# Kernel optimization log

Measured on AMD Instinct MI355X. Metric: run time of the kernel, lower is better.

The kernel has to match this reference:

```python
import jax, jax.numpy as jnp
import numpy as np

H = 512
TEMPERATURE = 1.0


def setup_inputs() -> dict:
    key = jax.random.key(0)
    ks = jax.random.split(key, 9)
    B, Q, S = 4, 64, 1024
    scale = 1.0 / np.sqrt(H)
    return {
        "query": jax.random.normal(ks[0], (B, Q, H), jnp.float32),
        "key_": jax.random.normal(ks[1], (B, S, H), jnp.float32),
        "value": jax.random.normal(ks[2], (B, S, H), jnp.float32),
        "Wq": jax.random.normal(ks[3], (H, H), jnp.float32) * scale,
        "bq": jax.random.normal(ks[4], (H,), jnp.float32) * 0.01,
        "Wk": jax.random.normal(ks[5], (H, H), jnp.float32) * scale,
        "bk": jax.random.normal(ks[6], (H,), jnp.float32) * 0.01,
        "we": jax.random.normal(ks[7], (H,), jnp.float32) * scale,
        "be": jax.random.normal(ks[8], (), jnp.float32) * 0.01,
    }


def reference(query, key_, value, Wq, bq, Wk, bk, we, be):
    # query: [B,Q,H], key_/value: [B,S,H]
    qp = jnp.einsum("bqd,dh->bqh", query, Wq) + bq          # [B,Q,H]
    kp = jnp.einsum("bsd,dh->bsh", key_, Wk) + bk           # [B,S,H]
    attn_sum = jnp.tanh(qp[:, :, None, :] + kp[:, None, :, :])  # [B,Q,S,H]
    scores = (jnp.einsum("bqsh,h->bqs", attn_sum, we) + be) / TEMPERATURE
    weights = jax.nn.softmax(scores, axis=-1)               # [B,Q,S]
    context = jnp.einsum("bqs,bsh->bqh", weights, value)    # [B,Q,H]
    return context, weights
```

## Files before the change

### kernel.cpp

```cpp
#include <hip/hip_runtime.h>


constexpr int kB = 4;
constexpr int kQ = 64;
constexpr int kS = 1024;
constexpr int kH = 512;

typedef short bf16x8 __attribute__((ext_vector_type(8)));
typedef float f32x4 __attribute__((ext_vector_type(4)));

__device__ __forceinline__ unsigned bf16rtn_bits(float x) {
  unsigned u = __float_as_uint(x);
  u += 0x7FFFu + ((u >> 16) & 1u);
  return u;
}

__global__ __launch_bounds__(256) void convert_all(
    const float* __restrict__ Wk, const float* __restrict__ Wq,
    const float* __restrict__ key_, const float* __restrict__ query,
    unsigned short* __restrict__ Bhi, unsigned short* __restrict__ Blo,
    unsigned short* __restrict__ Xhi, unsigned short* __restrict__ Xlo) {
  __shared__ __align__(16) unsigned short LHi[128 * 40];
  __shared__ __align__(16) unsigned short LLo[128 * 40];
  const int bid = blockIdx.x;
  const int t = threadIdx.x;
  if (bid < 256) {
    const int gid = bid * 256 + t;
    const int c = gid & 63;
    const int g = (gid >> 6) & 3;
    const int kt = (gid >> 8) & 15;
    const int ct = (gid >> 12) & 7;
    const int mat = gid >> 15;
    const float* W = mat ? Wq : Wk;
    const float* src = W + (size_t)(kt * 32 + g * 8) * kH + ct * 64 + c;
    bf16x8 hv, lv;
#pragma unroll
    for (int j = 0; j < 8; j++) {
      float x = src[(size_t)j * kH];
      unsigned u = bf16rtn_bits(x);
      float hf = __uint_as_float(u & 0xFFFF0000u);
      unsigned v = bf16rtn_bits(x - hf);
      hv[j] = (short)(u >> 16);
      lv[j] = (short)(v >> 16);
    }
    *(bf16x8*)(Bhi + (size_t)gid * 8) = hv;
    *(bf16x8*)(Blo + (size_t)gid * 8) = lv;
    return;
  }
  const int xb = bid - 256;
  const int kt = xb & 15;
  const int rt = xb >> 4;
  const float* X = (rt < 32) ? (key_ + (size_t)rt * 128 * kH)
                             : (query + (size_t)(rt - 32) * 128 * kH);
  const int r = t >> 1, c0 = (t & 1) * 16;
  const float* src = X + (size_t)r * kH + kt * 32 + c0;
  bf16x8 hv0, hv1, lv0, lv1;
#pragma unroll
  for (int i = 0; i < 16; i++) {
    float x = src[i];
    unsigned u = bf16rtn_bits(x);
    float hf = __uint_as_float(u & 0xFFFF0000u);
    unsigned v = bf16rtn_bits(x - hf);
    if (i < 8) { hv0[i] = (short)(u >> 16); lv0[i] = (short)(v >> 16); }
    else       { hv1[i - 8] = (short)(u >> 16); lv1[i - 8] = (short)(v >> 16); }
  }
  *(bf16x8*)&LHi[r * 40 + c0] = hv0;
  *(bf16x8*)&LHi[r * 40 + c0 + 8] = hv1;
  *(bf16x8*)&LLo[r * 40 + c0] = lv0;
  *(bf16x8*)&LLo[r * 40 + c0 + 8] = lv1;
  __syncthreads();
  const size_t obase = (size_t)(rt * 16 + kt) * 512 * 8;
#pragma unroll
  for (int p = 0; p < 2; p++) {
    const int s = t + p * 256;
    const int rr = s & 127, g = s >> 7;
    *(uint4*)(Xhi + obase + (size_t)s * 8) = *(const uint4*)&LHi[rr * 40 + g * 8];
    *(uint4*)(Xlo + obase + (size_t)s * 8) = *(const uint4*)&LLo[rr * 40 + g * 8];
  }
}

__global__ __launch_bounds__(512) void proj_mfma(
    const unsigned short* __restrict__ Xhi, const unsigned short* __restrict__ Xlo,
    const unsigned short* __restrict__ Bhi, const unsigned short* __restrict__ Blo,
    const float* __restrict__ bk, const float* __restrict__ bq,
    float* __restrict__ Ek, float* __restrict__ Eq) {
  __shared__ __align__(16) unsigned short AhiL[2][4096];
  __shared__ __align__(16) unsigned short AloL[2][4096];
  __shared__ __align__(16) unsigned short BhiL[2][2048];
  __shared__ __align__(16) unsigned short BloL[2][2048];

  const int ct = blockIdx.x;
  const int rt = blockIdx.y;
  const int mat = (rt >= 32) ? 1 : 0;
  const float* bias = mat ? bq : bk;
  float* Y = mat ? (Eq + (size_t)(rt - 32) * 128 * kH)
                 : (Ek + (size_t)rt * 128 * kH);

  const int t = threadIdx.x;
  const unsigned short* ah_src = Xhi + ((size_t)(rt * 16) * 512 + t) * 8;
  const unsigned short* al_src = Xlo + ((size_t)(rt * 16) * 512 + t) * 8;
  const int bslot = t & 255;
  const unsigned short* b_src =
      ((t < 256) ? Bhi : Blo) + ((size_t)((mat * 8 + ct) * 16) * 256 + bslot) * 8;

  uint4 pah, pal, pb;
  auto gload = [&](int kt2) {
    pah = *(const uint4*)(ah_src + (size_t)kt2 * 512 * 8);
    pal = *(const uint4*)(al_src + (size_t)kt2 * 512 * 8);
    pb = *(const uint4*)(b_src + (size_t)kt2 * 256 * 8);
  };
  auto lwrite = [&](int buf) {
    *(uint4*)&AhiL[buf][t * 8] = pah;
    *(uint4*)&AloL[buf][t * 8] = pal;
    if (t < 256) *(uint4*)&BhiL[buf][bslot * 8] = pb;
    else         *(uint4*)&BloL[buf][bslot * 8] = pb;
  };

  const int l = t & 63, lg = l >> 4, lr = l & 15;
  const int wv = t >> 6, wm = wv & 3, wn = wv >> 2;

  f32x4 acc[2][2];
#pragma unroll
  for (int m = 0; m < 2; m++)
#pragma unroll
    for (int n = 0; n < 2; n++) acc[m][n] = {0.f, 0.f, 0.f, 0.f};

  gload(0);
  lwrite(0);
  __syncthreads();

  for (int kt2 = 0; kt2 < 16; kt2++) {
    if (kt2 < 15) gload(kt2 + 1);

    const unsigned short* Ah = AhiL[kt2 & 1];
    const unsigned short* Al = AloL[kt2 & 1];
    const unsigned short* Bh = BhiL[kt2 & 1];
    const unsigned short* Bl = BloL[kt2 & 1];
    bf16x8 ah[2], al[2], bh[2], bl[2];
#pragma unroll
    for (int m = 0; m < 2; m++) {
      const int off = (lg * 128 + wm * 32 + m * 16 + lr) * 8;
      ah[m] = *(const bf16x8*)(Ah + off);
      al[m] = *(const bf16x8*)(Al + off);
    }
#pragma unroll
    for (int n = 0; n < 2; n++) {
      const int off = (lg * 64 + wn * 32 + n * 16 + lr) * 8;
      bh[n] = *(const bf16x8*)(Bh + off);
      bl[n] = *(const bf16x8*)(Bl + off);
    }
#pragma unroll
    for (int m = 0; m < 2; m++)
#pragma unroll
      for (int n = 0; n < 2; n++) {
        acc[m][n] = __builtin_amdgcn_mfma_f32_16x16x32_bf16(ah[m], bh[n], acc[m][n], 0, 0, 0);
        acc[m][n] = __builtin_amdgcn_mfma_f32_16x16x32_bf16(al[m], bh[n], acc[m][n], 0, 0, 0);
        acc[m][n] = __builtin_amdgcn_mfma_f32_16x16x32_bf16(ah[m], bl[n], acc[m][n], 0, 0, 0);
      }

    if (kt2 < 15) {
      __syncthreads();
      lwrite((kt2 + 1) & 1);
      __syncthreads();
    }
  }

  const int col0 = ct * 64 + wn * 32 + lr;
  const float b0 = bias[col0];
  const float b1 = bias[col0 + 16];
#pragma unroll
  for (int m = 0; m < 2; m++) {
    const int row0 = wm * 32 + m * 16 + lg * 4;
#pragma unroll
    for (int jj = 0; jj < 4; jj++) {
      float* y = Y + (size_t)(row0 + jj) * kH;
      y[col0]      = __expf(2.f * (acc[m][0][jj] + b0));
      y[col0 + 16] = __expf(2.f * (acc[m][1][jj] + b1));
    }
  }
}

__global__ __launch_bounds__(256) void score_kernel(
    const float* __restrict__ Eq, const float* __restrict__ Ek,
    const float* __restrict__ we, float* __restrict__ sraw) {
  __shared__ __align__(16) float EkL[2][64 * 64];

  const int qt = blockIdx.x, st = blockIdx.y, b = blockIdx.z;
  const int t = threadIdx.x, lane = t & 63;
  const int wvu = __builtin_amdgcn_readfirstlane(t >> 6);
  const int s0 = st * 64;
  const int q0g = b * kQ + qt * 8;
  const int qA = wvu * 2;

  const float4* we4 = (const float4*)we;
  float4 u0 = we4[lane * 2], u1 = we4[lane * 2 + 1];
  float wsum = u0.x + u0.y + u0.z + u0.w + u1.x + u1.y + u1.z + u1.w;
#pragma unroll
  for (int off = 32; off; off >>= 1) wsum += __shfl_xor(wsum, off);

  const float4* qa4 = (const float4*)(Eq + (size_t)(q0g + qA) * kH);
  const float4* qb4 = (const float4*)(Eq + (size_t)(q0g + qA + 1) * kH);

  const int er = t >> 4;
  const int ej = t & 15;
  const float* ekg = Ek + (size_t)(b * kS + s0 + er) * kH + ej * 4;
  float4 pk[4];
  auto gload = [&](int c) {
#pragma unroll
    for (int i = 0; i < 4; i++)
      pk[i] = *(const float4*)(ekg + (size_t)(16 * i) * kH + c * 64);
  };
  auto lwrite = [&](int buf) {
#pragma unroll
    for (int i = 0; i < 4; i++) {
      const int row = er + 16 * i;
      *(float4*)(&EkL[buf][row * 64 + ((ej ^ (row & 15)) << 2)]) = pk[i];
    }
  };

  gload(0);
  lwrite(0);
  __syncthreads();

  float accA = 0.f, accB = 0.f;
  const int sw = lane & 15;

  for (int c = 0; c < 8; c++) {
    if (c < 7) gload(c + 1);
    const float* ekb = &EkL[c & 1][lane * 64];
#pragma unroll 4
    for (int g = 0; g < 16; g++) {
      float4 ek = *(const float4*)(ekb + ((g ^ sw) << 2));
      float4 w = we4[c * 16 + g];
      float4 qa = qa4[c * 16 + g];
      float4 qb = qb4[c * 16 + g];
      {
        float a1 = fmaf(qa.x, ek.x, 1.f), b1 = fmaf(qa.y, ek.y, 1.f);
        float n1 = fmaf(w.y, a1, w.x * b1);
        accA = fmaf(n1, __builtin_amdgcn_rcpf(a1 * b1), accA);
        float a2 = fmaf(qa.z, ek.z, 1.f), b2 = fmaf(qa.w, ek.w, 1.f);
        float n2 = fmaf(w.w, a2, w.z * b2);
        accA = fmaf(n2, __builtin_amdgcn_rcpf(a2 * b2), accA);
      }
      {
        float a1 = fmaf(qb.x, ek.x, 1.f), b1 = fmaf(qb.y, ek.y, 1.f);
        float n1 = fmaf(w.y, a1, w.x * b1);
        accB = fmaf(n1, __builtin_amdgcn_rcpf(a1 * b1), accB);
        float a2 = fmaf(qb.z, ek.z, 1.f), b2 = fmaf(qb.w, ek.w, 1.f);
        float n2 = fmaf(w.w, a2, w.z * b2);
        accB = fmaf(n2, __builtin_amdgcn_rcpf(a2 * b2), accB);
      }
    }
    if (c < 7) {
      __syncthreads();
      lwrite((c + 1) & 1);
      __syncthreads();
    }
  }

  sraw[(size_t)(q0g + qA + 0) * kS + s0 + lane] = fmaf(-2.f, accA, wsum);
  sraw[(size_t)(q0g + qA + 1) * kS + s0 + lane] = fmaf(-2.f, accB, wsum);
}

__global__ __launch_bounds__(256) void ctx_fused(
    const float* __restrict__ sraw, const float* __restrict__ value,
    float* __restrict__ wout, float* __restrict__ ctx) {
  __shared__ __align__(16) float wt[4][1024];
  __shared__ __align__(16) float parts[4][4][128];
  const int bid = blockIdx.x;
  const int qc = bid >> 4, b = (bid >> 2) & 3, hc = bid & 3;
  const int t = threadIdx.x, wv = t >> 6, lane = t & 63;
  const int grow = b * kQ + qc * 4 + wv;

  const float4* row4 = (const float4*)(sraw + (size_t)grow * kS);
  float4 v[4];
#pragma unroll
  for (int j = 0; j < 4; j++) v[j] = row4[lane + 64 * j];
  float m = -1e30f;
#pragma unroll
  for (int j = 0; j < 4; j++)
    m = fmaxf(m, fmaxf(fmaxf(v[j].x, v[j].y), fmaxf(v[j].z, v[j].w)));
#pragma unroll
  for (int off = 32; off; off >>= 1) m = fmaxf(m, __shfl_xor(m, off));
  float sum = 0.f;
#pragma unroll
  for (int j = 0; j < 4; j++) {
    v[j].x = __expf(v[j].x - m); v[j].y = __expf(v[j].y - m);
    v[j].z = __expf(v[j].z - m); v[j].w = __expf(v[j].w - m);
    sum += v[j].x + v[j].y + v[j].z + v[j].w;
  }
#pragma unroll
  for (int off = 32; off; off >>= 1) sum += __shfl_xor(sum, off);
  const float inv = 1.f / sum;
  float4* wrow = (float4*)&wt[wv][0];
  float4* gw = (float4*)(wout + (size_t)grow * kS);
#pragma unroll
  for (int j = 0; j < 4; j++) {
    v[j].x *= inv; v[j].y *= inv; v[j].z *= inv; v[j].w *= inv;
    wrow[lane + 64 * j] = v[j];
    if (hc == 0) gw[lane + 64 * j] = v[j];
  }
  __syncthreads();

  const float* vbase =
      value + ((size_t)b * kS + wv * 256) * kH + hc * 128 + lane * 2;
  float2 acc[4];
#pragma unroll
  for (int q = 0; q < 4; q++) acc[q] = {0.f, 0.f};
#pragma unroll 2
  for (int s4 = 0; s4 < 64; s4++) {
    float4 wq[4];
#pragma unroll
    for (int q = 0; q < 4; q++)
      wq[q] = *(const float4*)&wt[q][wv * 256 + s4 * 4];
#pragma unroll
    for (int u = 0; u < 4; u++) {
      const float2 vv = *(const float2*)(vbase + (size_t)(s4 * 4 + u) * kH);
      const float w0 = ((const float*)&wq[0])[u];
      const float w1 = ((const float*)&wq[1])[u];
      const float w2 = ((const float*)&wq[2])[u];
      const float w3 = ((const float*)&wq[3])[u];
      acc[0].x = fmaf(w0, vv.x, acc[0].x); acc[0].y = fmaf(w0, vv.y, acc[0].y);
      acc[1].x = fmaf(w1, vv.x, acc[1].x); acc[1].y = fmaf(w1, vv.y, acc[1].y);
      acc[2].x = fmaf(w2, vv.x, acc[2].x); acc[2].y = fmaf(w2, vv.y, acc[2].y);
      acc[3].x = fmaf(w3, vv.x, acc[3].x); acc[3].y = fmaf(w3, vv.y, acc[3].y);
    }
  }
#pragma unroll
  for (int q = 0; q < 4; q++)
    *(float2*)&parts[wv][q][lane * 2] = acc[q];
  __syncthreads();

  const int q = t >> 6, hp = t & 63;
  float2 r = {0.f, 0.f};
#pragma unroll
  for (int w = 0; w < 4; w++) {
    const float2 p2 = *(const float2*)&parts[w][q][hp * 2];
    r.x += p2.x; r.y += p2.y;
  }
  *(float2*)(ctx + (size_t)(b * kQ + qc * 4 + q) * kH + hc * 128 + hp * 2) = r;
}

extern "C" void kernel_launch(void* const* d_in, const int* in_sizes, int n_in,
                              void* d_out, int out_size, void* d_ws,
                              size_t ws_size, hipStream_t stream) {
  const float* query = (const float*)d_in[0];
  const float* key_  = (const float*)d_in[1];
  const float* value = (const float*)d_in[2];
  const float* Wq    = (const float*)d_in[3];
  const float* bq    = (const float*)d_in[4];
  const float* Wk    = (const float*)d_in[5];
  const float* bk    = (const float*)d_in[6];
  const float* we    = (const float*)d_in[7];

  float* ctx  = (float*)d_out;
  float* wout = (float*)d_out + (size_t)kB * kQ * kH;

  float* Eq = (float*)d_ws;
  float* Ek = Eq + (size_t)kB * kQ * kH;
  unsigned short* Bhi =
      (unsigned short*)((char*)d_ws + (size_t)(kB * kQ * kH + kB * kS * kH) * 4);
  unsigned short* Blo = Bhi + (size_t)2 * 8 * 16 * 256 * 8;
  unsigned short* Xhi = Blo + (size_t)2 * 8 * 16 * 256 * 8;
  unsigned short* Xlo = Xhi + (size_t)34 * 16 * 512 * 8;
  float* sraw = (float*)(Xlo + (size_t)34 * 16 * 512 * 8);

  convert_all<<<800, 256, 0, stream>>>(Wk, Wq, key_, query, Bhi, Blo, Xhi, Xlo);
  proj_mfma<<<dim3(8, 34), 512, 0, stream>>>(Xhi, Xlo, Bhi, Blo, bk, bq, Ek, Eq);
  score_kernel<<<dim3(8, 16, 4), 256, 0, stream>>>(Eq, Ek, we, sraw);
  ctx_fused<<<256, 256, 0, stream>>>(sraw, value, wout, ctx);
}
```

Before: 148.4 us.

## Use direct global-to-LDS loads and smaller row tiles in projection GEMM

The projection kernel now stages tiles with global_load_lds straight into shared memory, so register staging and one barrier per iteration go away. Row tiles shrink from 128 to 64 with 256-thread blocks, doubling the grid to 544 blocks for better CU coverage. Block IDs are remapped so neighbouring blocks share column tiles, which should help L2 reuse. In exchange, B tiles are loaded twice as often overall, and the remaining barrier may not fully cover async LDS write completion.

```diff
diff --git a/kernel.cpp b/kernel.cpp
--- a/kernel.cpp
+++ b/kernel.cpp
@@ -13,6 +13,12 @@
   unsigned u = __float_as_uint(x);
   u += 0x7FFFu + ((u >> 16) & 1u);
   return u;
+}
+
+__device__ __forceinline__ void glds16(const void* g, void* l) {
+  __builtin_amdgcn_global_load_lds(
+      (__attribute__((address_space(1))) void*)(g),
+      (__attribute__((address_space(3))) void*)(l), 16, 0, 0);
 }
 
 __global__ __launch_bounds__(256) void convert_all(
@@ -79,45 +85,51 @@
   }
 }
 
-__global__ __launch_bounds__(512) void proj_mfma(
+__global__ __launch_bounds__(256) void proj_mfma(
     const unsigned short* __restrict__ Xhi, const unsigned short* __restrict__ Xlo,
     const unsigned short* __restrict__ Bhi, const unsigned short* __restrict__ Blo,
     const float* __restrict__ bk, const float* __restrict__ bq,
     float* __restrict__ Ek, float* __restrict__ Eq) {
-  __shared__ __align__(16) unsigned short AhiL[2][4096];
-  __shared__ __align__(16) unsigned short AloL[2][4096];
+  __shared__ __align__(16) unsigned short AhiL[2][2048];
+  __shared__ __align__(16) unsigned short AloL[2][2048];
   __shared__ __align__(16) unsigned short BhiL[2][2048];
   __shared__ __align__(16) unsigned short BloL[2][2048];
 
-  const int ct = blockIdx.x;
-  const int rt = blockIdx.y;
-  const int mat = (rt >= 32) ? 1 : 0;
+  const int bid = blockIdx.y * 8 + blockIdx.x;
+  int ct, rt;
+  if (bid < 512) {
+    ct = (bid >> 3) & 7;
+    rt = (bid & 7) + 8 * (bid >> 6);
+  } else {
+    const int tb = bid - 512;
+    ct = tb >> 2;
+    rt = 64 + (tb & 3);
+  }
+
+  const int mat = (rt >= 64) ? 1 : 0;
   const float* bias = mat ? bq : bk;
-  float* Y = mat ? (Eq + (size_t)(rt - 32) * 128 * kH)
-                 : (Ek + (size_t)rt * 128 * kH);
+  float* Y = mat ? (Eq + (size_t)(rt - 64) * 64 * kH)
+                 : (Ek + (size_t)rt * 64 * kH);
 
   const int t = threadIdx.x;
-  const unsigned short* ah_src = Xhi + ((size_t)(rt * 16) * 512 + t) * 8;
-  const unsigned short* al_src = Xlo + ((size_t)(rt * 16) * 512 + t) * 8;
-  const int bslot = t & 255;
-  const unsigned short* b_src =
-      ((t < 256) ? Bhi : Blo) + ((size_t)((mat * 8 + ct) * 16) * 256 + bslot) * 8;
-
-  uint4 pah, pal, pb;
-  auto gload = [&](int kt2) {
-    pah = *(const uint4*)(ah_src + (size_t)kt2 * 512 * 8);
-    pal = *(const uint4*)(al_src + (size_t)kt2 * 512 * 8);
-    pb = *(const uint4*)(b_src + (size_t)kt2 * 256 * 8);
+  const int rt128 = rt >> 1, hhalf = rt & 1;
+  const int ga_slot = ((t >> 6) << 7) + (hhalf << 6) + (t & 63);
+  const unsigned short* gah = Xhi + ((size_t)(rt128 * 16) * 512 + ga_slot) * 8;
+  const unsigned short* gal = Xlo + ((size_t)(rt128 * 16) * 512 + ga_slot) * 8;
+  const unsigned short* gbh = Bhi + (((size_t)(mat * 8 + ct) * 16) * 256 + t) * 8;
+  const unsigned short* gbl = Blo + (((size_t)(mat * 8 + ct) * 16) * 256 + t) * 8;
+
+  auto stage = [&](int buf, int kt2) {
+    glds16(gah + (size_t)kt2 * 512 * 8, &AhiL[buf][t * 8]);
+    glds16(gal + (size_t)kt2 * 512 * 8, &AloL[buf][t * 8]);
+    glds16(gbh + (size_t)kt2 * 256 * 8, &BhiL[buf][t * 8]);
+    glds16(gbl + (size_t)kt2 * 256 * 8, &BloL[buf][t * 8]);
   };
-  auto lwrite = [&](int buf) {
-    *(uint4*)&AhiL[buf][t * 8] = pah;
-    *(uint4*)&AloL[buf][t * 8] = pal;
-    if (t < 256) *(uint4*)&BhiL[buf][bslot * 8] = pb;
-    else         *(uint4*)&BloL[buf][bslot * 8] = pb;
-  };
 
   const int l = t & 63, lg = l >> 4, lr = l & 15;
-  const int wv = t >> 6, wm = wv & 3, wn = wv >> 2;
+  const int wv = t >> 6, wm = wv >> 1, wn = wv & 1;
+  const int oa0 = (lg * 64 + wm * 32 + lr) * 8;
+  const int ob0 = (lg * 64 + wn * 32 + lr) * 8;
 
   f32x4 acc[2][2];
 #pragma unroll
@@ -125,29 +137,27 @@
 #pragma unroll
     for (int n = 0; n < 2; n++) acc[m][n] = {0.f, 0.f, 0.f, 0.f};
 
-  gload(0);
-  lwrite(0);
-  __syncthreads();
-
+  stage(0, 0);
+  __syncthreads();
+
+  int buf = 0;
   for (int kt2 = 0; kt2 < 16; kt2++) {
-    if (kt2 < 15) gload(kt2 + 1);
-
-    const unsigned short* Ah = AhiL[kt2 & 1];
-    const unsigned short* Al = AloL[kt2 & 1];
-    const unsigned short* Bh = BhiL[kt2 & 1];
-    const unsigned short* Bl = BloL[kt2 & 1];
+    if (kt2 < 15) stage(buf ^ 1, kt2 + 1);
+
+    const unsigned short* Ah = AhiL[buf];
+    const unsigned short* Al = AloL[buf];
+    const unsigned short* Bh = BhiL[buf];
+    const unsigned short* Bl = BloL[buf];
     bf16x8 ah[2], al[2], bh[2], bl[2];
 #pragma unroll
     for (int m = 0; m < 2; m++) {
-      const int off = (lg * 128 + wm * 32 + m * 16 + lr) * 8;
-      ah[m] = *(const bf16x8*)(Ah + off);
-      al[m] = *(const bf16x8*)(Al + off);
+      ah[m] = *(const bf16x8*)(Ah + oa0 + m * 128);
+      al[m] = *(const bf16x8*)(Al + oa0 + m * 128);
     }
 #pragma unroll
     for (int n = 0; n < 2; n++) {
-      const int off = (lg * 64 + wn * 32 + n * 16 + lr) * 8;
-      bh[n] = *(const bf16x8*)(Bh + off);
-      bl[n] = *(const bf16x8*)(Bl + off);
+      bh[n] = *(const bf16x8*)(Bh + ob0 + n * 128);
+      bl[n] = *(const bf16x8*)(Bl + ob0 + n * 128);
     }
 #pragma unroll
     for (int m = 0; m < 2; m++)
@@ -158,11 +168,8 @@
         acc[m][n] = __builtin_amdgcn_mfma_f32_16x16x32_bf16(ah[m], bl[n], acc[m][n], 0, 0, 0);
       }
 
-    if (kt2 < 15) {
-      __syncthreads();
-      lwrite((kt2 + 1) & 1);
-      __syncthreads();
-    }
+    __syncthreads();
+    buf ^= 1;
   }
 
   const int col0 = ct * 64 + wn * 32 + lr;
@@ -366,7 +373,7 @@
   float* sraw = (float*)(Xlo + (size_t)34 * 16 * 512 * 8);
 
   convert_all<<<800, 256, 0, stream>>>(Wk, Wq, key_, query, Bhi, Blo, Xhi, Xlo);
-  proj_mfma<<<dim3(8, 34), 512, 0, stream>>>(Xhi, Xlo, Bhi, Blo, bk, bq, Ek, Eq);
+  proj_mfma<<<dim3(8, 68), 256, 0, stream>>>(Xhi, Xlo, Bhi, Blo, bk, bq, Ek, Eq);
   score_kernel<<<dim3(8, 16, 4), 256, 0, stream>>>(Eq, Ek, we, sraw);
   ctx_fused<<<256, 256, 0, stream>>>(sraw, value, wout, ctx);
 }
```

New measurement: 149.3 us. Within noise of the previous version (+0.6%).
